# Performance work log

Measured on AMD Instinct MI355X. Metric: run time of the kernel, lower is better.

Reference implementation:

```python
import jax, jax.numpy as jnp
import numpy as np

B, S = 4096, 256
D = 32  # output_size // 4


def setup_inputs() -> dict:
    key = jax.random.key(0)
    ks = jax.random.split(key, 32)
    # continuous features
    cont_p = jax.random.normal(ks[0], (B, S, 3), dtype=jnp.float32)
    cont_c = jax.random.normal(ks[1], (B, S, 2), dtype=jnp.float32)
    # categorical features, per-column vocab sizes from Embedding tables
    vocabs_p = [2, 2, 2, 11, 34]
    cat_p = jnp.stack([
        jax.random.randint(ks[2 + i], (B, S), 0, v, dtype=jnp.int32)
        for i, v in enumerate(vocabs_p)], axis=2)
    vocabs_c = [19, 31]
    cat_c = jnp.stack([
        jax.random.randint(ks[7 + i], (B, S), 0, v, dtype=jnp.int32)
        for i, v in enumerate(vocabs_c)], axis=2)
    lengths = jax.random.randint(ks[9], (B,), 1, S + 1, dtype=jnp.int32)

    def lin(k, fan_in, fan_out):
        bound = 1.0 / np.sqrt(fan_in)
        kw, kb = jax.random.split(k)
        w = jax.random.uniform(kw, (fan_in, fan_out), jnp.float32, -bound, bound)
        b = jax.random.uniform(kb, (fan_out,), jnp.float32, -bound, bound)
        return w, b

    w_p1, b_p1 = lin(ks[10], 3, D)
    w_p2, b_p2 = lin(ks[11], D, D)
    w_c1, b_c1 = lin(ks[12], 2, D)
    w_c2, b_c2 = lin(ks[13], D, D)
    emb_gender = jax.random.normal(ks[14], (2, D), dtype=jnp.float32)
    emb_korean = jax.random.normal(ks[15], (2, D), dtype=jnp.float32)
    emb_primary = jax.random.normal(ks[16], (2, D), dtype=jnp.float32)
    emb_job = jax.random.normal(ks[17], (11, D), dtype=jnp.float32)
    emb_rep = jax.random.normal(ks[18], (34, D), dtype=jnp.float32)
    emb_place = jax.random.normal(ks[19], (19, D), dtype=jnp.float32)
    emb_add = jax.random.normal(ks[20], (31, D), dtype=jnp.float32)
    w_fc1, b_fc1 = lin(ks[21], 128, 64)
    w_fc2, b_fc2 = lin(ks[22], 64, 2)

    return dict(cont_p=cont_p, cont_c=cont_c, cat_p=cat_p, cat_c=cat_c,
                lengths=lengths,
                w_p1=w_p1, b_p1=b_p1, w_p2=w_p2, b_p2=b_p2,
                w_c1=w_c1, b_c1=b_c1, w_c2=w_c2, b_c2=b_c2,
                emb_gender=emb_gender, emb_korean=emb_korean,
                emb_primary=emb_primary, emb_job=emb_job, emb_rep=emb_rep,
                emb_place=emb_place, emb_add=emb_add,
                w_fc1=w_fc1, b_fc1=b_fc1, w_fc2=w_fc2, b_fc2=b_fc2)


def reference(cont_p, cont_c, cat_p, cat_c, lengths,
              w_p1, b_p1, w_p2, b_p2, w_c1, b_c1, w_c2, b_c2,
              emb_gender, emb_korean, emb_primary, emb_job, emb_rep,
              emb_place, emb_add, w_fc1, b_fc1, w_fc2, b_fc2):
    # small per-token MLPs on continuous features -> [B,S,D]
    hp = jax.nn.relu(cont_p @ w_p1 + b_p1) @ w_p2 + b_p2
    hc = jax.nn.relu(cont_c @ w_c1 + b_c1) @ w_c2 + b_c2
    # multi-table embedding lookups, averaged per group -> [B,S,D]
    ep = (emb_gender[cat_p[:, :, 0]] + emb_korean[cat_p[:, :, 1]] +
          emb_primary[cat_p[:, :, 2]] + emb_job[cat_p[:, :, 3]] +
          emb_rep[cat_p[:, :, 4]]) / 5.0
    ec = (emb_place[cat_c[:, :, 0]] + emb_add[cat_c[:, :, 1]]) / 2.0
    # concat order matches torch: (cat_p, cat_c, cont_p, cont_c) -> [B,S,128]
    x = jnp.concatenate([ep, ec, hp, hc], axis=2)
    # ragged mean pool over first lengths[i] positions (masked segment mean)
    mask = (jnp.arange(x.shape[1])[None, :] < lengths[:, None])
    pooled = jnp.sum(x * mask[:, :, None], axis=1) / lengths[:, None].astype(x.dtype)
    # head: relu(fc1) -> relu(fc2); dropout p=0.0 is identity
    h = jax.nn.relu(pooled @ w_fc1 + b_fc1)
    return jax.nn.relu(h @ w_fc2 + b_fc2)
```

## Files before the change

kernel.cpp:

```cpp
#include <hip/hip_runtime.h>


#define BDIM 256

__device__ __forceinline__ void gld16(const void* g, void* l) {
    __builtin_amdgcn_global_load_lds((__attribute__((address_space(1))) void*)g,
                                     (__attribute__((address_space(3))) void*)l,
                                     16, 0, 0);
}

__global__ __launch_bounds__(BDIM)
void mlpreg_kernel(const float* __restrict__ cont_p,
                   const float* __restrict__ cont_c,
                   const int* __restrict__ cat_p,
                   const int* __restrict__ cat_c,
                   const int* __restrict__ lengths,
                   const float* __restrict__ w_p1, const float* __restrict__ b_p1,
                   const float* __restrict__ w_p2, const float* __restrict__ b_p2,
                   const float* __restrict__ w_c1, const float* __restrict__ b_c1,
                   const float* __restrict__ w_c2, const float* __restrict__ b_c2,
                   const float* __restrict__ emb_g,  const float* __restrict__ emb_k,
                   const float* __restrict__ emb_pr, const float* __restrict__ emb_j,
                   const float* __restrict__ emb_r,  const float* __restrict__ emb_pl,
                   const float* __restrict__ emb_a,
                   const float* __restrict__ w_fc1, const float* __restrict__ b_fc1,
                   const float* __restrict__ w_fc2, const float* __restrict__ b_fc2,
                   float* __restrict__ out)
{
    constexpr int S = 256;
    __shared__ __align__(16) float sPc[4][192];
    __shared__ __align__(16) float sCc[4][128];
    __shared__ __align__(16) int   sKp[4][320];
    __shared__ int   hist[96];
    __shared__ float sAccW[4][64];
    __shared__ int   sSums[4][3];
    __shared__ float sPool[128];

    const int tid  = threadIdx.x;
    const int wid  = tid >> 6;
    const int lane = tid & 63;
    const int ch   = lane & 31, h = lane >> 5;
    const int b    = blockIdx.x;

    int L = lengths[b]; L = (L < 1) ? 1 : (L > S ? S : L);
    const float Lf = (float)L, invL = 1.0f / Lf;

    const int t0 = wid << 6;
    const int nt = (L - t0 < 64) ? (L - t0) : 64;

    if (tid < 96) hist[tid] = 0;

    if (nt > 0) {
        const char* gp = (const char*)(cont_p + (size_t)b * 768  + t0 * 3);
        const char* gc = (const char*)(cont_c + (size_t)b * 512  + t0 * 2);
        const char* gk = (const char*)(cat_p  + (size_t)b * 1280 + t0 * 5);
        const int lo = 16 * lane;
        const int bP = 12 * nt, bC = 8 * nt, bK = 20 * nt;
        if (lo < bP)        gld16(gp + lo,        (char*)sPc[wid]);
        if (lo < bC)        gld16(gc + lo,        (char*)sCc[wid]);
        if (lo < bK)        gld16(gk + lo,        (char*)sKp[wid]);
        if (1024 + lo < bK) gld16(gk + 1024 + lo, (char*)sKp[wid] + 1024);
    }
    int2 qc; qc.x = 0; qc.y = 0;
    if (lane < nt) qc = ((const int2*)(cat_c + (size_t)b * 512))[t0 + lane];

    const float wp0 = w_p1[ch], wp1v = w_p1[32 + ch], wp2v = w_p1[64 + ch], bp = b_p1[ch];
    const float wc0 = w_c1[ch], wc1v = w_c1[32 + ch], bc = b_c1[ch];
    float eg0 = 0, eg1 = 0, ek0 = 0, ek1 = 0, er0 = 0, er1 = 0;
    float bias2 = 0, bf1 = 0, bq0 = 0, bq1 = 0;
    float2 wf2; wf2.x = 0; wf2.y = 0;
    if (wid == 0) {
        eg0 = emb_g[ch];  eg1 = emb_g[32 + ch];
        ek0 = emb_k[ch];  ek1 = emb_k[32 + ch];
        er0 = emb_pr[ch]; er1 = emb_pr[32 + ch];
        bias2 = h ? b_c2[ch] : b_p2[ch];
        bf1 = b_fc1[lane];
        wf2 = *(const float2*)&w_fc2[2 * lane];
        bq0 = b_fc2[0]; bq1 = b_fc2[1];
    }

    __syncthreads();

    float aP = 0.f, aC = 0.f;
    if (nt > 0) {
        const int gf = nt >> 2;
        const int gh = (gf + 1) >> 1;
        const float4* tp4 = (const float4*)sPc[wid];
        const float4* tc4 = (const float4*)sCc[wid];
        #pragma unroll 4
        for (int i = 0; i < gh; ++i) {
            const int g = h ? gh + i : i;
            if (g < gf) {
                float4 a  = tp4[3 * g], bb = tp4[3 * g + 1], cc = tp4[3 * g + 2];
                float4 d  = tc4[2 * g], ee = tc4[2 * g + 1];
                float p0 = fmaxf(fmaf(a.x,  wp0, fmaf(a.y,  wp1v, fmaf(a.z,  wp2v, bp))), 0.f);
                float p1 = fmaxf(fmaf(a.w,  wp0, fmaf(bb.x, wp1v, fmaf(bb.y, wp2v, bp))), 0.f);
                float p2 = fmaxf(fmaf(bb.z, wp0, fmaf(bb.w, wp1v, fmaf(cc.x, wp2v, bp))), 0.f);
                float p3 = fmaxf(fmaf(cc.y, wp0, fmaf(cc.z, wp1v, fmaf(cc.w, wp2v, bp))), 0.f);
                aP += (p0 + p1) + (p2 + p3);
                float q0 = fmaxf(fmaf(d.x,  wc0, fmaf(d.y,  wc1v, bc)), 0.f);
                float q1 = fmaxf(fmaf(d.z,  wc0, fmaf(d.w,  wc1v, bc)), 0.f);
                float q2 = fmaxf(fmaf(ee.x, wc0, fmaf(ee.y, wc1v, bc)), 0.f);
                float q3 = fmaxf(fmaf(ee.z, wc0, fmaf(ee.w, wc1v, bc)), 0.f);
                aC += (q0 + q1) + (q2 + q3);
            }
        }
        const int rem = nt & 3;
        if (h == 0 && rem) {
            const float* tp = sPc[wid] + 12 * gf;
            const float* tc = sCc[wid] + 8 * gf;
            for (int r = 0; r < rem; ++r) {
                aP += fmaxf(fmaf(tp[3*r], wp0, fmaf(tp[3*r+1], wp1v, fmaf(tp[3*r+2], wp2v, bp))), 0.f);
                aC += fmaxf(fmaf(tc[2*r], wc0, fmaf(tc[2*r+1], wc1v, bc)), 0.f);
            }
        }
    }
    aP += __shfl_xor(aP, 32);
    aC += __shfl_xor(aC, 32);
    sAccW[wid][lane] = h ? aC : aP;

    int v0 = 0, v1 = 0, v2 = 0;
    if (lane < nt) {
        const int* kp = sKp[wid] + 5 * lane;
        v0 = kp[0]; v1 = kp[1]; v2 = kp[2];
        const int v3 = kp[3], v4 = kp[4];
        atomicAdd(&hist[v3], 1);
        atomicAdd(&hist[11 + v4], 1);
        atomicAdd(&hist[45 + qc.x], 1);
        atomicAdd(&hist[64 + qc.y], 1);
    }
    #pragma unroll
    for (int d = 32; d; d >>= 1) {
        v0 += __shfl_xor(v0, d); v1 += __shfl_xor(v1, d); v2 += __shfl_xor(v2, d);
    }
    if (lane == 0) { sSums[wid][0] = v0; sSums[wid][1] = v1; sSums[wid][2] = v2; }
    __syncthreads();

    if (wid == 0) {
        const int sg = sSums[0][0] + sSums[1][0] + sSums[2][0] + sSums[3][0];
        const int sk = sSums[0][1] + sSums[1][1] + sSums[2][1] + sSums[3][1];
        const int sp = sSums[0][2] + sSums[1][2] + sSums[2][2] + sSums[3][2];
        float A;
        {
            float fg = (float)sg, fk = (float)sk, fp = (float)sp;
            A = fmaf(Lf - fg, eg0, fg * eg1) + fmaf(Lf - fk, ek0, fk * ek1)
              + fmaf(Lf - fp, er0, fp * er1);
            A = h ? 0.f : A;
        }
        {
            const float* tA = h ? emb_pl : emb_j;
            const float* tB = h ? emb_a  : emb_r;
            const int nA = h ? 19 : 11;
            const int nT = h ? 50 : 45;
            const int hb = h ? 45 : 0;
            #pragma unroll 5
            for (int r = 0; r < nT; ++r) {
                const float* p = (r < nA) ? (tA + (r << 5)) : (tB + ((r - nA) << 5));
                A = fmaf((float)hist[hb + r], p[ch], A);
            }
            sPool[(h << 5) + ch] = A * (invL * (h ? 0.5f : 0.2f));
        }
        {
            const float* W2 = h ? w_c2 : w_p2;
            float vsum = 0.f;
            #pragma unroll 8
            for (int k = 0; k < 32; ++k) {
                const int a = (h << 5) + k;
                float ak = ((sAccW[0][a] + sAccW[1][a]) + (sAccW[2][a] + sAccW[3][a]));
                vsum = fmaf(ak, W2[(k << 5) + ch], vsum);
            }
            sPool[64 + (h << 5) + ch] = fmaf(invL, vsum, bias2);
        }
    }
    __syncthreads();

    if (wid == 0) {
        float x = bf1, y = 0.f;
        #pragma unroll 8
        for (int k = 0; k < 128; k += 2) {
            float w0 = w_fc1[(size_t)k * 64 + lane];
            float w1 = w_fc1[(size_t)(k + 1) * 64 + lane];
            float2 u = *(const float2*)&sPool[k];
            x = fmaf(u.x, w0, x); y = fmaf(u.y, w1, y);
        }
        float hv = fmaxf(x + y, 0.f);
        float q0 = hv * wf2.x, q1 = hv * wf2.y;
        #pragma unroll
        for (int d = 32; d; d >>= 1) {
            q0 += __shfl_xor(q0, d); q1 += __shfl_xor(q1, d);
        }
        if (lane == 0) {
            float2 o2;
            o2.x = fmaxf(q0 + bq0, 0.f);
            o2.y = fmaxf(q1 + bq1, 0.f);
            *(float2*)&out[(size_t)b * 2] = o2;
        }
    }
}

extern "C" void kernel_launch(void* const* d_in, const int* in_sizes, int n_in,
                              void* d_out, int out_size, void* d_ws, size_t ws_size,
                              hipStream_t stream) {
    const float* cont_p = (const float*)d_in[0];
    const float* cont_c = (const float*)d_in[1];
    const int*   cat_p  = (const int*)d_in[2];
    const int*   cat_c  = (const int*)d_in[3];
    const int*   lens   = (const int*)d_in[4];
    const float* w_p1   = (const float*)d_in[5];
    const float* b_p1   = (const float*)d_in[6];
    const float* w_p2   = (const float*)d_in[7];
    const float* b_p2   = (const float*)d_in[8];
    const float* w_c1   = (const float*)d_in[9];
    const float* b_c1   = (const float*)d_in[10];
    const float* w_c2   = (const float*)d_in[11];
    const float* b_c2   = (const float*)d_in[12];
    const float* emb_g  = (const float*)d_in[13];
    const float* emb_k  = (const float*)d_in[14];
    const float* emb_pr = (const float*)d_in[15];
    const float* emb_j  = (const float*)d_in[16];
    const float* emb_r  = (const float*)d_in[17];
    const float* emb_pl = (const float*)d_in[18];
    const float* emb_a  = (const float*)d_in[19];
    const float* w_fc1  = (const float*)d_in[20];
    const float* b_fc1  = (const float*)d_in[21];
    const float* w_fc2  = (const float*)d_in[22];
    const float* b_fc2  = (const float*)d_in[23];
    float* out = (float*)d_out;

    hipLaunchKernelGGL(mlpreg_kernel, dim3(4096), dim3(BDIM), 0, stream,
                       cont_p, cont_c, cat_p, cat_c, lens,
                       w_p1, b_p1, w_p2, b_p2, w_c1, b_c1, w_c2, b_c2,
                       emb_g, emb_k, emb_pr, emb_j, emb_r, emb_pl, emb_a,
                       w_fc1, b_fc1, w_fc2, b_fc2, out);
}
```

Measured before the change: 146.6 us.

## Spread per-block epilogue across all four waves with shared-memory atomics

The serial epilogue, which previously ran only on wave 0, is now split across all four waves. That epilogue covers the histogram-weighted embedding sums, the second-layer projection of the continuous MLPs and the fc1 matvec. Partial results are combined with LDS float atomics into sPool and a new sF buffer, at the cost of one extra barrier. The launch bounds also request 8 blocks per CU to limit register use. The aim is to shorten the tail latency of each block, at the cost of extra syncs and atomics and a float summation order that can differ from run to run.

```diff
diff --git a/kernel.cpp b/kernel.cpp
--- a/kernel.cpp
+++ b/kernel.cpp
@@ -9,7 +9,7 @@
                                      16, 0, 0);
 }
 
-__global__ __launch_bounds__(BDIM)
+__global__ __launch_bounds__(BDIM, 8)
 void mlpreg_kernel(const float* __restrict__ cont_p,
                    const float* __restrict__ cont_c,
                    const int* __restrict__ cat_p,
@@ -35,6 +35,7 @@
     __shared__ float sAccW[4][64];
     __shared__ int   sSums[4][3];
     __shared__ float sPool[128];
+    __shared__ float sF[4][64];
 
     const int tid  = threadIdx.x;
     const int wid  = tid >> 6;
@@ -48,7 +49,8 @@
     const int t0 = wid << 6;
     const int nt = (L - t0 < 64) ? (L - t0) : 64;
 
-    if (tid < 96) hist[tid] = 0;
+    if (tid < 96)  hist[tid] = 0;
+    if (tid < 128) sPool[tid] = 0.f;
 
     if (nt > 0) {
         const char* gp = (const char*)(cont_p + (size_t)b * 768  + t0 * 3);
@@ -136,54 +138,67 @@
     if (lane == 0) { sSums[wid][0] = v0; sSums[wid][1] = v1; sSums[wid][2] = v2; }
     __syncthreads();
 
+    {
+        float Ap = 0.f, Ac = 0.f;
+        if (wid == 0 && h == 0) {
+            const int sg = sSums[0][0] + sSums[1][0] + sSums[2][0] + sSums[3][0];
+            const int sk = sSums[0][1] + sSums[1][1] + sSums[2][1] + sSums[3][1];
+            const int sp = sSums[0][2] + sSums[1][2] + sSums[2][2] + sSums[3][2];
+            float fg = (float)sg, fk = (float)sk, fp = (float)sp;
+            Ap = fmaf(Lf - fg, eg0, fg * eg1) + fmaf(Lf - fk, ek0, fk * ek1)
+               + fmaf(Lf - fp, er0, fp * er1);
+        }
+        const int base = 24 * wid;
+        #pragma unroll
+        for (int r = 0; r < 12; ++r) {
+            const int rr = base + 2 * r + h;
+            if (rr < 95) {
+                const float* p;
+                if (rr < 11)      p = emb_j  + (rr << 5);
+                else if (rr < 45) p = emb_r  + ((rr - 11) << 5);
+                else if (rr < 64) p = emb_pl + ((rr - 45) << 5);
+                else              p = emb_a  + ((rr - 64) << 5);
+                const float t = (float)hist[rr];
+                const float wv = p[ch];
+                if (rr < 45) Ap = fmaf(t, wv, Ap);
+                else         Ac = fmaf(t, wv, Ac);
+            }
+        }
+        atomicAdd(&sPool[ch],      Ap * (invL * 0.2f));
+        atomicAdd(&sPool[32 + ch], Ac * (invL * 0.5f));
+    }
+
+    {
+        const float* W2 = h ? w_c2 : w_p2;
+        float partial = 0.f;
+        #pragma unroll
+        for (int k = 0; k < 8; ++k) {
+            const int kk = 8 * wid + k;
+            const int a = (h << 5) + kk;
+            const float ak = (sAccW[0][a] + sAccW[1][a]) + (sAccW[2][a] + sAccW[3][a]);
+            partial = fmaf(ak, W2[(kk << 5) + ch], partial);
+        }
+        float val = partial * invL;
+        if (wid == 0) val += bias2;
+        atomicAdd(&sPool[64 + (h << 5) + ch], val);
+    }
+    __syncthreads();
+
+    {
+        const int o = lane, q = wid;
+        float x = 0.f;
+        const int k0 = q << 5;
+        #pragma unroll 8
+        for (int k = 0; k < 32; ++k) {
+            x = fmaf(sPool[k0 + k], w_fc1[(size_t)(k0 + k) * 64 + o], x);
+        }
+        sF[q][o] = x;
+    }
+    __syncthreads();
+
     if (wid == 0) {
-        const int sg = sSums[0][0] + sSums[1][0] + sSums[2][0] + sSums[3][0];
-        const int sk = sSums[0][1] + sSums[1][1] + sSums[2][1] + sSums[3][1];
-        const int sp = sSums[0][2] + sSums[1][2] + sSums[2][2] + sSums[3][2];
-        float A;
-        {
-            float fg = (float)sg, fk = (float)sk, fp = (float)sp;
-            A = fmaf(Lf - fg, eg0, fg * eg1) + fmaf(Lf - fk, ek0, fk * ek1)
-              + fmaf(Lf - fp, er0, fp * er1);
-            A = h ? 0.f : A;
-        }
-        {
-            const float* tA = h ? emb_pl : emb_j;
-            const float* tB = h ? emb_a  : emb_r;
-            const int nA = h ? 19 : 11;
-            const int nT = h ? 50 : 45;
-            const int hb = h ? 45 : 0;
-            #pragma unroll 5
-            for (int r = 0; r < nT; ++r) {
-                const float* p = (r < nA) ? (tA + (r << 5)) : (tB + ((r - nA) << 5));
-                A = fmaf((float)hist[hb + r], p[ch], A);
-            }
-            sPool[(h << 5) + ch] = A * (invL * (h ? 0.5f : 0.2f));
-        }
-        {
-            const float* W2 = h ? w_c2 : w_p2;
-            float vsum = 0.f;
-            #pragma unroll 8
-            for (int k = 0; k < 32; ++k) {
-                const int a = (h << 5) + k;
-                float ak = ((sAccW[0][a] + sAccW[1][a]) + (sAccW[2][a] + sAccW[3][a]));
-                vsum = fmaf(ak, W2[(k << 5) + ch], vsum);
-            }
-            sPool[64 + (h << 5) + ch] = fmaf(invL, vsum, bias2);
-        }
-    }
-    __syncthreads();
-
-    if (wid == 0) {
-        float x = bf1, y = 0.f;
-        #pragma unroll 8
-        for (int k = 0; k < 128; k += 2) {
-            float w0 = w_fc1[(size_t)k * 64 + lane];
-            float w1 = w_fc1[(size_t)(k + 1) * 64 + lane];
-            float2 u = *(const float2*)&sPool[k];
-            x = fmaf(u.x, w0, x); y = fmaf(u.y, w1, y);
-        }
-        float hv = fmaxf(x + y, 0.f);
+        float x = (sF[0][lane] + sF[1][lane]) + (sF[2][lane] + sF[3][lane]) + bf1;
+        float hv = fmaxf(x, 0.f);
         float q0 = hv * wf2.x, q1 = hv * wf2.y;
         #pragma unroll
         for (int d = 32; d; d >>= 1) {
```

Result: slower. 157.2 us (+7.3%).
